# Kernel optimization log

Hardware: AMD Instinct MI355X
Metric: run time of the kernel (lower is better)

Reference implementation:

```python
import jax, jax.numpy as jnp
import numpy as np

N_NODES = 100000
N_EDGES = 3200000
IN_DIM = 32
HID = 64


def setup_inputs() -> dict:
    key = jax.random.key(0)
    ks = jax.random.split(key, 10)
    x = jax.random.normal(ks[0], (N_NODES, IN_DIM), dtype=jnp.float32)
    edge_index = jax.random.randint(ks[1], (2, N_EDGES), 0, N_NODES, dtype=jnp.int64)
    s = 0.1
    return {
        "x": x,
        "edge_index": edge_index,
        # SAGEConv layer 1: lin_l (neighbor path, with bias), lin_r (root path, no bias)
        "w1_l": jax.random.normal(ks[2], (HID, IN_DIM), dtype=jnp.float32) * s,
        "b1_l": jnp.zeros((HID,), dtype=jnp.float32),
        "w1_r": jax.random.normal(ks[3], (HID, IN_DIM), dtype=jnp.float32) * s,
        # SAGEConv layer 2
        "w2_l": jax.random.normal(ks[4], (HID, HID), dtype=jnp.float32) * s,
        "b2_l": jnp.zeros((HID,), dtype=jnp.float32),
        "w2_r": jax.random.normal(ks[5], (HID, HID), dtype=jnp.float32) * s,
        # final classifier Linear(hidden, 1)
        "w_cls": jax.random.normal(ks[6], (1, HID), dtype=jnp.float32) * s,
        "b_cls": jnp.zeros((1,), dtype=jnp.float32),
    }


def _sage_conv(h, src, dst, n_nodes, w_l, b_l, w_r):
    # mean-aggregate neighbor features (src -> dst), then lin_l(agg) + lin_r(h)
    msg = h[src]                                   # [E, F] gather
    agg = jax.ops.segment_sum(msg, dst, num_segments=n_nodes)
    cnt = jax.ops.segment_sum(jnp.ones((src.shape[0],), h.dtype), dst,
                              num_segments=n_nodes)
    mean = agg / jnp.maximum(cnt, 1.0)[:, None]    # [N, F]
    return mean @ w_l.T + b_l + h @ w_r.T


def reference(x, edge_index, w1_l, b1_l, w1_r, w2_l, b2_l, w2_r, w_cls, b_cls):
    src, dst = edge_index[0], edge_index[1]
    n = x.shape[0]
    h = _sage_conv(x, src, dst, n, w1_l, b1_l, w1_r)
    h = jax.nn.relu(h)  # dropout is identity at inference
    h = _sage_conv(h, src, dst, n, w2_l, b2_l, w2_r)
    h = jax.nn.relu(h)
    logits = h @ w_cls.T + b_cls                   # [N, 1]
    return jnp.squeeze(logits, -1)                 # [N]
```

## Files before the change

### kernel.cpp

```cpp
#include <hip/hip_runtime.h>

#define N_NODES 100000
#define N_EDGES 3200000
#define IN_DIM 32
#define HID 64
#define BSHIFT 8
#define BNODES 256
#define NB ((N_NODES + BNODES - 1) / BNODES)
#define NWG 256
#define CHUNK (N_EDGES / NWG)

typedef unsigned short u16;
typedef _Float16 h2 __attribute__((ext_vector_type(2)));
typedef _Float16 half8 __attribute__((ext_vector_type(8)));
typedef float float4v __attribute__((ext_vector_type(4)));

__device__ __forceinline__ h2 as_h2(unsigned u) {
  return __builtin_bit_cast(h2, u);
}
__device__ __forceinline__ unsigned as_u(h2 v) {
  return __builtin_bit_cast(unsigned, v);
}
__device__ __forceinline__ h2 shfl_xor_h2(h2 v, int m) {
  int i = __builtin_bit_cast(int, v);
  i = __shfl_xor(i, m, 64);
  return __builtin_bit_cast(h2, i);
}
__device__ __forceinline__ u16 f2h(float f) {
  _Float16 h = (_Float16)f;
  return __builtin_bit_cast(u16, h);
}
__device__ __forceinline__ unsigned scale_h2(unsigned u, float rinv) {
  h2 v = as_h2(u);
  h2 o;
  o.x = (_Float16)((float)v.x * rinv);
  o.y = (_Float16)((float)v.y * rinv);
  return as_u(o);
}

__global__ __launch_bounds__(256) void to_f16(
    const float* __restrict__ in, u16* __restrict__ outv, int n) {
  int i = blockIdx.x * 256 + threadIdx.x;
  if (i < n) outv[i] = f2h(in[i]);
}

__global__ __launch_bounds__(256) void prep_weights(
    const float* __restrict__ w1l, const float* __restrict__ w1r,
    const float* __restrict__ w2l, const float* __restrict__ w2r,
    u16* __restrict__ w1lf, u16* __restrict__ w1rf,
    u16* __restrict__ w2lf, u16* __restrict__ w2rf) {
  int i = blockIdx.x * 256 + threadIdx.x;
  if (i < HID * IN_DIM) {
    w1lf[i] = f2h(w1l[i]);
    w1rf[i] = f2h(w1r[i]);
  }
  if (i < HID * HID) {
    w2lf[i] = f2h(w2l[i]);
    w2rf[i] = f2h(w2r[i]);
  }
}

__global__ __launch_bounds__(256) void csr_count(
    const int* __restrict__ dst, int* __restrict__ counts) {
  __shared__ int h[NB];
  int w = blockIdx.x, tid = threadIdx.x;
  for (int i = tid; i < NB; i += 256) h[i] = 0;
  __syncthreads();
  int e0 = w * CHUNK;
  for (int i = tid; i < CHUNK; i += 256)
    atomicAdd(&h[dst[e0 + i] >> BSHIFT], 1);
  __syncthreads();
  for (int i = tid; i < NB; i += 256) counts[w * NB + i] = h[i];
}

__global__ __launch_bounds__(256) void csr_scan_w(
    int* __restrict__ counts, int* __restrict__ btot) {
  __shared__ int s[256];
  int b = blockIdx.x, tid = threadIdx.x;
  int v = counts[tid * NB + b];
  s[tid] = v;
  __syncthreads();
  for (int off = 1; off < 256; off <<= 1) {
    int t = (tid >= off) ? s[tid - off] : 0;
    __syncthreads();
    s[tid] += t;
    __syncthreads();
  }
  counts[tid * NB + b] = s[tid] - v;
  if (tid == 255) btot[b] = s[255];
}

__global__ __launch_bounds__(256) void csr_scan_b(
    const int* __restrict__ btot, int* __restrict__ bbase) {
  __shared__ int s[256];
  int tid = threadIdx.x;
  int g0 = tid * 2, g1 = tid * 2 + 1;
  int v0 = (g0 < NB) ? btot[g0] : 0;
  int v1 = (g1 < NB) ? btot[g1] : 0;
  int tsum = v0 + v1;
  s[tid] = tsum;
  __syncthreads();
  for (int off = 1; off < 256; off <<= 1) {
    int t = (tid >= off) ? s[tid - off] : 0;
    __syncthreads();
    s[tid] += t;
    __syncthreads();
  }
  int run = s[tid] - tsum;
  if (g0 < NB) bbase[g0] = run;
  if (g1 < NB) bbase[g1] = run + v0;
  if (tid == 0) bbase[NB] = N_EDGES;
}

__global__ __launch_bounds__(256) void csr_place(
    const int* __restrict__ src, const int* __restrict__ dst,
    const int* __restrict__ counts, const int* __restrict__ bbase,
    unsigned* __restrict__ staged) {
  __shared__ int cur[NB];
  int w = blockIdx.x, tid = threadIdx.x;
  for (int i = tid; i < NB; i += 256) cur[i] = bbase[i] + counts[w * NB + i];
  __syncthreads();
  int e0 = w * CHUNK;
  for (int i = tid; i < CHUNK; i += 256) {
    int d = dst[e0 + i];
    int b = d >> BSHIFT;
    int pos = atomicAdd(&cur[b], 1);
    staged[pos] = ((unsigned)src[e0 + i] << 8) | (unsigned)(d & (BNODES - 1));
  }
}

__global__ __launch_bounds__(256) void csr_fill(
    const unsigned* __restrict__ staged, const int* __restrict__ bbase,
    int* __restrict__ row_ptr, int* __restrict__ sorted_src) {
  __shared__ int s_cnt[BNODES];
  __shared__ int s_scan[BNODES];
  int b = blockIdx.x, tid = threadIdx.x;
  int n0 = b << BSHIFT;
  int beg = bbase[b], end = bbase[b + 1];
  s_cnt[tid] = 0;
  __syncthreads();
  for (int i = beg + tid; i < end; i += 256)
    atomicAdd(&s_cnt[staged[i] & (BNODES - 1)], 1);
  __syncthreads();
  int v = s_cnt[tid];
  s_scan[tid] = v;
  __syncthreads();
  for (int off = 1; off < BNODES; off <<= 1) {
    int t = (tid >= off) ? s_scan[tid - off] : 0;
    __syncthreads();
    s_scan[tid] += t;
    __syncthreads();
  }
  int excl = s_scan[tid] - v;
  int node = n0 + tid;
  if (node < N_NODES) row_ptr[node] = beg + excl;
  if (b == 0 && tid == 0) row_ptr[N_NODES] = N_EDGES;
  s_cnt[tid] = excl;
  __syncthreads();
  for (int i = beg + tid; i < end; i += 256) {
    unsigned p = staged[i];
    int r = atomicAdd(&s_cnt[p & (BNODES - 1)], 1);
    sorted_src[beg + r] = (int)(p >> 8);
  }
}

#define F1 72
__global__ __launch_bounds__(256) void layer1_fused(
    const u16* __restrict__ xh, const int* __restrict__ row_ptr,
    const int* __restrict__ sorted_src, const u16* __restrict__ w_lf,
    const float* __restrict__ b_l, const u16* __restrict__ w_rf,
    u16* __restrict__ h1h) {
  __shared__ __align__(16) u16 s_feat[16 * F1];

  int tid = threadIdx.x;
  int w = tid >> 6, lane = tid & 63;
  int q = lane & 3, g = lane >> 2;

  for (int m = 0; m < 4; ++m) {
    int nl = 4 * w + m;
    int node = blockIdx.x * 16 + nl;
    int rs = row_ptr[node];
    int deg = row_ptr[node + 1] - rs;
    h2 a0{}, a1{}, a2{}, a3{}, b0{}, b1{}, b2{}, b3{};
    int kk = g;
    for (; kk + 16 < deg; kk += 32) {
      int s0 = sorted_src[rs + kk];
      int s1 = sorted_src[rs + kk + 16];
      uint4 u0 = *(const uint4*)&xh[s0 * IN_DIM + 8 * q];
      uint4 u1 = *(const uint4*)&xh[s1 * IN_DIM + 8 * q];
      a0 += as_h2(u0.x); a1 += as_h2(u0.y); a2 += as_h2(u0.z); a3 += as_h2(u0.w);
      b0 += as_h2(u1.x); b1 += as_h2(u1.y); b2 += as_h2(u1.z); b3 += as_h2(u1.w);
    }
    if (kk < deg) {
      int s0 = sorted_src[rs + kk];
      uint4 u0 = *(const uint4*)&xh[s0 * IN_DIM + 8 * q];
      a0 += as_h2(u0.x); a1 += as_h2(u0.y); a2 += as_h2(u0.z); a3 += as_h2(u0.w);
    }
    a0 += b0; a1 += b1; a2 += b2; a3 += b3;
#pragma unroll
    for (int off = 4; off < 64; off <<= 1) {
      a0 += shfl_xor_h2(a0, off);
      a1 += shfl_xor_h2(a1, off);
      a2 += shfl_xor_h2(a2, off);
      a3 += shfl_xor_h2(a3, off);
    }
    if (g == 0) {
      float rinv = 1.0f / fmaxf((float)deg, 1.0f);
      uint4 o;
      o.x = scale_h2(as_u(a0), rinv);
      o.y = scale_h2(as_u(a1), rinv);
      o.z = scale_h2(as_u(a2), rinv);
      o.w = scale_h2(as_u(a3), rinv);
      *(uint4*)&s_feat[nl * F1 + 8 * q] = o;
    }
  }
  {
    int nm = lane >> 4, q2 = lane & 15;
    int nl = 4 * w + nm;
    int node = blockIdx.x * 16 + nl;
    unsigned ux = *(const unsigned*)&xh[node * IN_DIM + 2 * q2];
    *(unsigned*)&s_feat[nl * F1 + IN_DIM + 2 * q2] = ux;
  }
  __syncthreads();

  int q16 = lane & 15, g4 = lane >> 4;
  int j = 16 * w + q16;
  half8 b0f = *(const half8*)&w_lf[j * IN_DIM + 8 * g4];
  half8 b1f = *(const half8*)&w_rf[j * IN_DIM + 8 * g4];
  half8 a0f = *(const half8*)&s_feat[q16 * F1 + 8 * g4];
  half8 a1f = *(const half8*)&s_feat[q16 * F1 + 32 + 8 * g4];
  float4v acc = {};
  acc = __builtin_amdgcn_mfma_f32_16x16x32_f16(a0f, b0f, acc, 0, 0, 0);
  acc = __builtin_amdgcn_mfma_f32_16x16x32_f16(a1f, b1f, acc, 0, 0, 0);
  float bj = b_l[j];
#pragma unroll
  for (int reg = 0; reg < 4; ++reg) {
    int nl = 4 * g4 + reg;
    float v = fmaxf(acc[reg] + bj, 0.0f);
    h1h[(blockIdx.x * 16 + nl) * HID + j] = f2h(v);
  }
}

#define F2 136
__global__ __launch_bounds__(256) void layer2_fused(
    const u16* __restrict__ h1h, const int* __restrict__ row_ptr,
    const int* __restrict__ sorted_src, const u16* __restrict__ w_lf,
    const float* __restrict__ b_l, const u16* __restrict__ w_rf,
    const float* __restrict__ wc, const float* __restrict__ bc,
    float* __restrict__ out) {
  __shared__ __align__(16) u16 s_feat[16 * F2];
  __shared__ float s_out[16];

  int tid = threadIdx.x;
  if (tid < 16) s_out[tid] = bc[0];

  int w = tid >> 6, lane = tid & 63;
  int q = lane & 7, g = lane >> 3;

  for (int m = 0; m < 4; ++m) {
    int nl = 4 * w + m;
    int node = blockIdx.x * 16 + nl;
    int rs = row_ptr[node];
    int deg = row_ptr[node + 1] - rs;
    h2 a0{}, a1{}, a2{}, a3{}, b0{}, b1{}, b2{}, b3{};
    int kk = g;
    for (; kk + 8 < deg; kk += 16) {
      int s0 = sorted_src[rs + kk];
      int s1 = sorted_src[rs + kk + 8];
      uint4 u0 = *(const uint4*)&h1h[s0 * HID + 8 * q];
      uint4 u1 = *(const uint4*)&h1h[s1 * HID + 8 * q];
      a0 += as_h2(u0.x); a1 += as_h2(u0.y); a2 += as_h2(u0.z); a3 += as_h2(u0.w);
      b0 += as_h2(u1.x); b1 += as_h2(u1.y); b2 += as_h2(u1.z); b3 += as_h2(u1.w);
    }
    if (kk < deg) {
      int s0 = sorted_src[rs + kk];
      uint4 u0 = *(const uint4*)&h1h[s0 * HID + 8 * q];
      a0 += as_h2(u0.x); a1 += as_h2(u0.y); a2 += as_h2(u0.z); a3 += as_h2(u0.w);
    }
    a0 += b0; a1 += b1; a2 += b2; a3 += b3;
#pragma unroll
    for (int off = 8; off < 64; off <<= 1) {
      a0 += shfl_xor_h2(a0, off);
      a1 += shfl_xor_h2(a1, off);
      a2 += shfl_xor_h2(a2, off);
      a3 += shfl_xor_h2(a3, off);
    }
    if (g == 0) {
      float rinv = 1.0f / fmaxf((float)deg, 1.0f);
      uint4 o;
      o.x = scale_h2(as_u(a0), rinv);
      o.y = scale_h2(as_u(a1), rinv);
      o.z = scale_h2(as_u(a2), rinv);
      o.w = scale_h2(as_u(a3), rinv);
      *(uint4*)&s_feat[nl * F2 + 8 * q] = o;
    }
  }
  {
    int nm = lane >> 4, q2 = lane & 15;
    int nl = 4 * w + nm;
    int node = blockIdx.x * 16 + nl;
    uint2 uh = *(const uint2*)&h1h[node * HID + 4 * q2];
    *(uint2*)&s_feat[nl * F2 + HID + 4 * q2] = uh;
  }
  __syncthreads();

  int q16 = lane & 15, g4 = lane >> 4;
  int j = 16 * w + q16;
  half8 bf0 = *(const half8*)&w_lf[j * HID + 8 * g4];
  half8 bf1 = *(const half8*)&w_lf[j * HID + 32 + 8 * g4];
  half8 bf2 = *(const half8*)&w_rf[j * HID + 8 * g4];
  half8 bf3 = *(const half8*)&w_rf[j * HID + 32 + 8 * g4];
  float4v acc = {};
  acc = __builtin_amdgcn_mfma_f32_16x16x32_f16(
      *(const half8*)&s_feat[q16 * F2 + 8 * g4], bf0, acc, 0, 0, 0);
  acc = __builtin_amdgcn_mfma_f32_16x16x32_f16(
      *(const half8*)&s_feat[q16 * F2 + 32 + 8 * g4], bf1, acc, 0, 0, 0);
  acc = __builtin_amdgcn_mfma_f32_16x16x32_f16(
      *(const half8*)&s_feat[q16 * F2 + 64 + 8 * g4], bf2, acc, 0, 0, 0);
  acc = __builtin_amdgcn_mfma_f32_16x16x32_f16(
      *(const half8*)&s_feat[q16 * F2 + 96 + 8 * g4], bf3, acc, 0, 0, 0);
  float bj = b_l[j];
  float wcj = wc[j];
#pragma unroll
  for (int reg = 0; reg < 4; ++reg) {
    float v = fmaxf(acc[reg] + bj, 0.0f) * wcj;
    v += __shfl_xor(v, 1, 64);
    v += __shfl_xor(v, 2, 64);
    v += __shfl_xor(v, 4, 64);
    v += __shfl_xor(v, 8, 64);
    if (q16 == 0) atomicAdd(&s_out[4 * g4 + reg], v);
  }
  __syncthreads();
  if (tid < 16) out[blockIdx.x * 16 + tid] = s_out[tid];
}

extern "C" void kernel_launch(void* const* d_in, const int* in_sizes, int n_in,
                              void* d_out, int out_size, void* d_ws, size_t ws_size,
                              hipStream_t stream) {
  const float* x   = (const float*)d_in[0];
  const int*   ei  = (const int*)d_in[1];
  const float* w1l = (const float*)d_in[2];
  const float* b1l = (const float*)d_in[3];
  const float* w1r = (const float*)d_in[4];
  const float* w2l = (const float*)d_in[5];
  const float* b2l = (const float*)d_in[6];
  const float* w2r = (const float*)d_in[7];
  const float* wc  = (const float*)d_in[8];
  const float* bc  = (const float*)d_in[9];
  float* out = (float*)d_out;

  const int* src = ei;
  const int* dst = ei + N_EDGES;

  char* ws = (char*)d_ws;
  int*      row_ptr    = (int*)(ws + 0);
  int*      counts     = (int*)(ws + 400128);
  int*      btot       = (int*)(ws + 800768);
  int*      bbase      = (int*)(ws + 802560);
  unsigned* staged     = (unsigned*)(ws + 804352);
  int*      sorted_src = (int*)(ws + 13604352);
  u16*      xh         = (u16*)(ws + 26404352);
  u16*      h1h        = (u16*)(ws + 32804352);
  u16*      w1lf       = (u16*)(ws + 45604352);
  u16*      w1rf       = (u16*)(ws + 45608448);
  u16*      w2lf       = (u16*)(ws + 45612544);
  u16*      w2rf       = (u16*)(ws + 45620736);

  to_f16<<<(N_NODES * IN_DIM + 255) / 256, 256, 0, stream>>>(x, xh,
                                                             N_NODES * IN_DIM);
  prep_weights<<<(HID * HID + 255) / 256, 256, 0, stream>>>(
      w1l, w1r, w2l, w2r, w1lf, w1rf, w2lf, w2rf);
  csr_count<<<NWG, 256, 0, stream>>>(dst, counts);
  csr_scan_w<<<NB, 256, 0, stream>>>(counts, btot);
  csr_scan_b<<<1, 256, 0, stream>>>(btot, bbase);
  csr_place<<<NWG, 256, 0, stream>>>(src, dst, counts, bbase, staged);
  csr_fill<<<NB, 256, 0, stream>>>(staged, bbase, row_ptr, sorted_src);
  layer1_fused<<<N_NODES / 16, 256, 0, stream>>>(xh, row_ptr, sorted_src,
                                                 w1lf, b1l, w1rf, h1h);
  layer2_fused<<<N_NODES / 16, 256, 0, stream>>>(h1h, row_ptr, sorted_src,
                                                 w2lf, b2l, w2rf, wc, bc, out);
}
```

Baseline: 199.0 us.

## Interleave four nodes' neighbor gathers per wave and hoist weight loads

Each wave now gathers neighbors for its four nodes together in one loop bounded by the maximum degree, instead of handling the nodes one after another. This puts up to four independent gathers in flight per iteration, which raises memory-level parallelism and removes the serial per-node loop latency. Weight and bias loads are moved before the gather so they overlap with it, and launch bounds request 8 blocks per CU. The cost is more live registers for 16 accumulators, plus idle lanes on the divergent branches when the four degrees are unequal.

```diff
diff --git a/kernel.cpp b/kernel.cpp
--- a/kernel.cpp
+++ b/kernel.cpp
@@ -165,7 +165,7 @@
 }
 
 #define F1 72
-__global__ __launch_bounds__(256) void layer1_fused(
+__global__ __launch_bounds__(256, 8) void layer1_fused(
     const u16* __restrict__ xh, const int* __restrict__ row_ptr,
     const int* __restrict__ sorted_src, const u16* __restrict__ w_lf,
     const float* __restrict__ b_l, const u16* __restrict__ w_rf,
@@ -176,43 +176,75 @@
   int w = tid >> 6, lane = tid & 63;
   int q = lane & 3, g = lane >> 2;
 
-  for (int m = 0; m < 4; ++m) {
-    int nl = 4 * w + m;
-    int node = blockIdx.x * 16 + nl;
-    int rs = row_ptr[node];
-    int deg = row_ptr[node + 1] - rs;
-    h2 a0{}, a1{}, a2{}, a3{}, b0{}, b1{}, b2{}, b3{};
-    int kk = g;
-    for (; kk + 16 < deg; kk += 32) {
-      int s0 = sorted_src[rs + kk];
-      int s1 = sorted_src[rs + kk + 16];
-      uint4 u0 = *(const uint4*)&xh[s0 * IN_DIM + 8 * q];
-      uint4 u1 = *(const uint4*)&xh[s1 * IN_DIM + 8 * q];
-      a0 += as_h2(u0.x); a1 += as_h2(u0.y); a2 += as_h2(u0.z); a3 += as_h2(u0.w);
-      b0 += as_h2(u1.x); b1 += as_h2(u1.y); b2 += as_h2(u1.z); b3 += as_h2(u1.w);
-    }
-    if (kk < deg) {
-      int s0 = sorted_src[rs + kk];
-      uint4 u0 = *(const uint4*)&xh[s0 * IN_DIM + 8 * q];
-      a0 += as_h2(u0.x); a1 += as_h2(u0.y); a2 += as_h2(u0.z); a3 += as_h2(u0.w);
-    }
-    a0 += b0; a1 += b1; a2 += b2; a3 += b3;
+  int q16 = lane & 15, g4 = lane >> 4;
+  int j = 16 * w + q16;
+  half8 b0f = *(const half8*)&w_lf[j * IN_DIM + 8 * g4];
+  half8 b1f = *(const half8*)&w_rf[j * IN_DIM + 8 * g4];
+  float bj = b_l[j];
+
+  int nbase = blockIdx.x * 16 + 4 * w;
+  int r0 = row_ptr[nbase + 0], r1 = row_ptr[nbase + 1];
+  int r2 = row_ptr[nbase + 2], r3 = row_ptr[nbase + 3];
+  int r4 = row_ptr[nbase + 4];
+  int d0 = r1 - r0, d1 = r2 - r1, d2 = r3 - r2, d3 = r4 - r3;
+  int dmax = max(max(d0, d1), max(d2, d3));
+
+  h2 A0{}, A1{}, A2{}, A3{};
+  h2 B0{}, B1{}, B2{}, B3{};
+  h2 C0{}, C1{}, C2{}, C3{};
+  h2 D0{}, D1{}, D2{}, D3{};
+  for (int kk = g; kk < dmax; kk += 16) {
+    if (kk < d0) {
+      int s = sorted_src[r0 + kk];
+      uint4 u = *(const uint4*)&xh[s * IN_DIM + 8 * q];
+      A0 += as_h2(u.x); A1 += as_h2(u.y); A2 += as_h2(u.z); A3 += as_h2(u.w);
+    }
+    if (kk < d1) {
+      int s = sorted_src[r1 + kk];
+      uint4 u = *(const uint4*)&xh[s * IN_DIM + 8 * q];
+      B0 += as_h2(u.x); B1 += as_h2(u.y); B2 += as_h2(u.z); B3 += as_h2(u.w);
+    }
+    if (kk < d2) {
+      int s = sorted_src[r2 + kk];
+      uint4 u = *(const uint4*)&xh[s * IN_DIM + 8 * q];
+      C0 += as_h2(u.x); C1 += as_h2(u.y); C2 += as_h2(u.z); C3 += as_h2(u.w);
+    }
+    if (kk < d3) {
+      int s = sorted_src[r3 + kk];
+      uint4 u = *(const uint4*)&xh[s * IN_DIM + 8 * q];
+      D0 += as_h2(u.x); D1 += as_h2(u.y); D2 += as_h2(u.z); D3 += as_h2(u.w);
+    }
+  }
 #pragma unroll
-    for (int off = 4; off < 64; off <<= 1) {
-      a0 += shfl_xor_h2(a0, off);
-      a1 += shfl_xor_h2(a1, off);
-      a2 += shfl_xor_h2(a2, off);
-      a3 += shfl_xor_h2(a3, off);
-    }
-    if (g == 0) {
-      float rinv = 1.0f / fmaxf((float)deg, 1.0f);
-      uint4 o;
-      o.x = scale_h2(as_u(a0), rinv);
-      o.y = scale_h2(as_u(a1), rinv);
-      o.z = scale_h2(as_u(a2), rinv);
-      o.w = scale_h2(as_u(a3), rinv);
-      *(uint4*)&s_feat[nl * F1 + 8 * q] = o;
-    }
+  for (int off = 4; off < 64; off <<= 1) {
+    A0 += shfl_xor_h2(A0, off); A1 += shfl_xor_h2(A1, off);
+    A2 += shfl_xor_h2(A2, off); A3 += shfl_xor_h2(A3, off);
+    B0 += shfl_xor_h2(B0, off); B1 += shfl_xor_h2(B1, off);
+    B2 += shfl_xor_h2(B2, off); B3 += shfl_xor_h2(B3, off);
+    C0 += shfl_xor_h2(C0, off); C1 += shfl_xor_h2(C1, off);
+    C2 += shfl_xor_h2(C2, off); C3 += shfl_xor_h2(C3, off);
+    D0 += shfl_xor_h2(D0, off); D1 += shfl_xor_h2(D1, off);
+    D2 += shfl_xor_h2(D2, off); D3 += shfl_xor_h2(D3, off);
+  }
+  if (g == 0) {
+    int nl = 4 * w;
+    float ri0 = 1.0f / fmaxf((float)d0, 1.0f);
+    float ri1 = 1.0f / fmaxf((float)d1, 1.0f);
+    float ri2 = 1.0f / fmaxf((float)d2, 1.0f);
+    float ri3 = 1.0f / fmaxf((float)d3, 1.0f);
+    uint4 o;
+    o.x = scale_h2(as_u(A0), ri0); o.y = scale_h2(as_u(A1), ri0);
+    o.z = scale_h2(as_u(A2), ri0); o.w = scale_h2(as_u(A3), ri0);
+    *(uint4*)&s_feat[(nl + 0) * F1 + 8 * q] = o;
+    o.x = scale_h2(as_u(B0), ri1); o.y = scale_h2(as_u(B1), ri1);
+    o.z = scale_h2(as_u(B2), ri1); o.w = scale_h2(as_u(B3), ri1);
+    *(uint4*)&s_feat[(nl + 1) * F1 + 8 * q] = o;
+    o.x = scale_h2(as_u(C0), ri2); o.y = scale_h2(as_u(C1), ri2);
+    o.z = scale_h2(as_u(C2), ri2); o.w = scale_h2(as_u(C3), ri2);
+    *(uint4*)&s_feat[(nl + 2) * F1 + 8 * q] = o;
+    o.x = scale_h2(as_u(D0), ri3); o.y = scale_h2(as_u(D1), ri3);
+    o.z = scale_h2(as_u(D2), ri3); o.w = scale_h2(as_u(D3), ri3);
+    *(uint4*)&s_feat[(nl + 3) * F1 + 8 * q] = o;
   }
   {
     int nm = lane >> 4, q2 = lane & 15;
@@ -223,16 +255,11 @@
   }
   __syncthreads();
 
-  int q16 = lane & 15, g4 = lane >> 4;
-  int j = 16 * w + q16;
-  half8 b0f = *(const half8*)&w_lf[j * IN_DIM + 8 * g4];
-  half8 b1f = *(const half8*)&w_rf[j * IN_DIM + 8 * g4];
   half8 a0f = *(const half8*)&s_feat[q16 * F1 + 8 * g4];
   half8 a1f = *(const half8*)&s_feat[q16 * F1 + 32 + 8 * g4];
   float4v acc = {};
   acc = __builtin_amdgcn_mfma_f32_16x16x32_f16(a0f, b0f, acc, 0, 0, 0);
   acc = __builtin_amdgcn_mfma_f32_16x16x32_f16(a1f, b1f, acc, 0, 0, 0);
-  float bj = b_l[j];
 #pragma unroll
   for (int reg = 0; reg < 4; ++reg) {
     int nl = 4 * g4 + reg;
@@ -242,7 +269,7 @@
 }
 
 #define F2 136
-__global__ __launch_bounds__(256) void layer2_fused(
+__global__ __launch_bounds__(256, 8) void layer2_fused(
     const u16* __restrict__ h1h, const int* __restrict__ row_ptr,
     const int* __restrict__ sorted_src, const u16* __restrict__ w_lf,
     const float* __restrict__ b_l, const u16* __restrict__ w_rf,
@@ -257,43 +284,78 @@
   int w = tid >> 6, lane = tid & 63;
   int q = lane & 7, g = lane >> 3;
 
-  for (int m = 0; m < 4; ++m) {
-    int nl = 4 * w + m;
-    int node = blockIdx.x * 16 + nl;
-    int rs = row_ptr[node];
-    int deg = row_ptr[node + 1] - rs;
-    h2 a0{}, a1{}, a2{}, a3{}, b0{}, b1{}, b2{}, b3{};
-    int kk = g;
-    for (; kk + 8 < deg; kk += 16) {
-      int s0 = sorted_src[rs + kk];
-      int s1 = sorted_src[rs + kk + 8];
-      uint4 u0 = *(const uint4*)&h1h[s0 * HID + 8 * q];
-      uint4 u1 = *(const uint4*)&h1h[s1 * HID + 8 * q];
-      a0 += as_h2(u0.x); a1 += as_h2(u0.y); a2 += as_h2(u0.z); a3 += as_h2(u0.w);
-      b0 += as_h2(u1.x); b1 += as_h2(u1.y); b2 += as_h2(u1.z); b3 += as_h2(u1.w);
-    }
-    if (kk < deg) {
-      int s0 = sorted_src[rs + kk];
-      uint4 u0 = *(const uint4*)&h1h[s0 * HID + 8 * q];
-      a0 += as_h2(u0.x); a1 += as_h2(u0.y); a2 += as_h2(u0.z); a3 += as_h2(u0.w);
-    }
-    a0 += b0; a1 += b1; a2 += b2; a3 += b3;
+  int q16 = lane & 15, g4 = lane >> 4;
+  int j = 16 * w + q16;
+  half8 bf0 = *(const half8*)&w_lf[j * HID + 8 * g4];
+  half8 bf1 = *(const half8*)&w_lf[j * HID + 32 + 8 * g4];
+  half8 bf2 = *(const half8*)&w_rf[j * HID + 8 * g4];
+  half8 bf3 = *(const half8*)&w_rf[j * HID + 32 + 8 * g4];
+  float bj = b_l[j];
+  float wcj = wc[j];
+
+  int nbase = blockIdx.x * 16 + 4 * w;
+  int r0 = row_ptr[nbase + 0], r1 = row_ptr[nbase + 1];
+  int r2 = row_ptr[nbase + 2], r3 = row_ptr[nbase + 3];
+  int r4 = row_ptr[nbase + 4];
+  int d0 = r1 - r0, d1 = r2 - r1, d2 = r3 - r2, d3 = r4 - r3;
+  int dmax = max(max(d0, d1), max(d2, d3));
+
+  h2 A0{}, A1{}, A2{}, A3{};
+  h2 B0{}, B1{}, B2{}, B3{};
+  h2 C0{}, C1{}, C2{}, C3{};
+  h2 D0{}, D1{}, D2{}, D3{};
+  for (int kk = g; kk < dmax; kk += 8) {
+    if (kk < d0) {
+      int s = sorted_src[r0 + kk];
+      uint4 u = *(const uint4*)&h1h[s * HID + 8 * q];
+      A0 += as_h2(u.x); A1 += as_h2(u.y); A2 += as_h2(u.z); A3 += as_h2(u.w);
+    }
+    if (kk < d1) {
+      int s = sorted_src[r1 + kk];
+      uint4 u = *(const uint4*)&h1h[s * HID + 8 * q];
+      B0 += as_h2(u.x); B1 += as_h2(u.y); B2 += as_h2(u.z); B3 += as_h2(u.w);
+    }
+    if (kk < d2) {
+      int s = sorted_src[r2 + kk];
+      uint4 u = *(const uint4*)&h1h[s * HID + 8 * q];
+      C0 += as_h2(u.x); C1 += as_h2(u.y); C2 += as_h2(u.z); C3 += as_h2(u.w);
+    }
+    if (kk < d3) {
+      int s = sorted_src[r3 + kk];
+      uint4 u = *(const uint4*)&h1h[s * HID + 8 * q];
+      D0 += as_h2(u.x); D1 += as_h2(u.y); D2 += as_h2(u.z); D3 += as_h2(u.w);
+    }
+  }
 #pragma unroll
-    for (int off = 8; off < 64; off <<= 1) {
-      a0 += shfl_xor_h2(a0, off);
-      a1 += shfl_xor_h2(a1, off);
-      a2 += shfl_xor_h2(a2, off);
-      a3 += shfl_xor_h2(a3, off);
-    }
-    if (g == 0) {
-      float rinv = 1.0f / fmaxf((float)deg, 1.0f);
-      uint4 o;
-      o.x = scale_h2(as_u(a0), rinv);
-      o.y = scale_h2(as_u(a1), rinv);
-      o.z = scale_h2(as_u(a2), rinv);
-      o.w = scale_h2(as_u(a3), rinv);
-      *(uint4*)&s_feat[nl * F2 + 8 * q] = o;
-    }
+  for (int off = 8; off < 64; off <<= 1) {
+    A0 += shfl_xor_h2(A0, off); A1 += shfl_xor_h2(A1, off);
+    A2 += shfl_xor_h2(A2, off); A3 += shfl_xor_h2(A3, off);
+    B0 += shfl_xor_h2(B0, off); B1 += shfl_xor_h2(B1, off);
+    B2 += shfl_xor_h2(B2, off); B3 += shfl_xor_h2(B3, off);
+    C0 += shfl_xor_h2(C0, off); C1 += shfl_xor_h2(C1, off);
+    C2 += shfl_xor_h2(C2, off); C3 += shfl_xor_h2(C3, off);
+    D0 += shfl_xor_h2(D0, off); D1 += shfl_xor_h2(D1, off);
+    D2 += shfl_xor_h2(D2, off); D3 += shfl_xor_h2(D3, off);
+  }
+  if (g == 0) {
+    int nl = 4 * w;
+    float ri0 = 1.0f / fmaxf((float)d0, 1.0f);
+    float ri1 = 1.0f / fmaxf((float)d1, 1.0f);
+    float ri2 = 1.0f / fmaxf((float)d2, 1.0f);
+    float ri3 = 1.0f / fmaxf((float)d3, 1.0f);
+    uint4 o;
+    o.x = scale_h2(as_u(A0), ri0); o.y = scale_h2(as_u(A1), ri0);
+    o.z = scale_h2(as_u(A2), ri0); o.w = scale_h2(as_u(A3), ri0);
+    *(uint4*)&s_feat[(nl + 0) * F2 + 8 * q] = o;
+    o.x = scale_h2(as_u(B0), ri1); o.y = scale_h2(as_u(B1), ri1);
+    o.z = scale_h2(as_u(B2), ri1); o.w = scale_h2(as_u(B3), ri1);
+    *(uint4*)&s_feat[(nl + 1) * F2 + 8 * q] = o;
+    o.x = scale_h2(as_u(C0), ri2); o.y = scale_h2(as_u(C1), ri2);
+    o.z = scale_h2(as_u(C2), ri2); o.w = scale_h2(as_u(C3), ri2);
+    *(uint4*)&s_feat[(nl + 2) * F2 + 8 * q] = o;
+    o.x = scale_h2(as_u(D0), ri3); o.y = scale_h2(as_u(D1), ri3);
+    o.z = scale_h2(as_u(D2), ri3); o.w = scale_h2(as_u(D3), ri3);
+    *(uint4*)&s_feat[(nl + 3) * F2 + 8 * q] = o;
   }
   {
     int nm = lane >> 4, q2 = lane & 15;
@@ -304,12 +366,6 @@
   }
   __syncthreads();
 
-  int q16 = lane & 15, g4 = lane >> 4;
-  int j = 16 * w + q16;
-  half8 bf0 = *(const half8*)&w_lf[j * HID + 8 * g4];
-  half8 bf1 = *(const half8*)&w_lf[j * HID + 32 + 8 * g4];
-  half8 bf2 = *(const half8*)&w_rf[j * HID + 8 * g4];
-  half8 bf3 = *(const half8*)&w_rf[j * HID + 32 + 8 * g4];
   float4v acc = {};
   acc = __builtin_amdgcn_mfma_f32_16x16x32_f16(
       *(const half8*)&s_feat[q16 * F2 + 8 * g4], bf0, acc, 0, 0, 0);
@@ -319,8 +375,6 @@
       *(const half8*)&s_feat[q16 * F2 + 64 + 8 * g4], bf2, acc, 0, 0, 0);
   acc = __builtin_amdgcn_mfma_f32_16x16x32_f16(
       *(const half8*)&s_feat[q16 * F2 + 96 + 8 * g4], bf3, acc, 0, 0, 0);
-  float bj = b_l[j];
-  float wcj = wc[j];
 #pragma unroll
   for (int reg = 0; reg < 4; ++reg) {
     float v = fmaxf(acc[reg] + bj, 0.0f) * wcj;
```

Result: slower. 214.4 us (+7.8%).

## Use finer CSR buckets and more partition workgroups in edge sort

Applied to the files above, without the earlier changes.

The CSR construction now uses 64-node buckets (1563 buckets) and 1024 partitioning workgroups instead of 256-node buckets and 256 workgroups. The two scan kernels are reworked so each thread handles 4 workgroups or 8 buckets, and csr_fill only uses 64 threads for its per-node scan. The intent is more parallelism in the count and place passes, with smaller, better-spread fill blocks. The cost is a larger counts matrix, more LDS atomics per workgroup, and a relocated workspace layout.

```diff
diff --git a/kernel.cpp b/kernel.cpp
--- a/kernel.cpp
+++ b/kernel.cpp
@@ -4,10 +4,10 @@
 #define N_EDGES 3200000
 #define IN_DIM 32
 #define HID 64
-#define BSHIFT 8
-#define BNODES 256
+#define BSHIFT 6
+#define BNODES 64
 #define NB ((N_NODES + BNODES - 1) / BNODES)
-#define NWG 256
+#define NWG 1024
 #define CHUNK (N_EDGES / NWG)
 
 typedef unsigned short u16;
@@ -77,8 +77,14 @@
     int* __restrict__ counts, int* __restrict__ btot) {
   __shared__ int s[256];
   int b = blockIdx.x, tid = threadIdx.x;
-  int v = counts[tid * NB + b];
-  s[tid] = v;
+  int v[4];
+  int tsum = 0;
+#pragma unroll
+  for (int i = 0; i < 4; ++i) {
+    v[i] = counts[(4 * tid + i) * NB + b];
+    tsum += v[i];
+  }
+  s[tid] = tsum;
   __syncthreads();
   for (int off = 1; off < 256; off <<= 1) {
     int t = (tid >= off) ? s[tid - off] : 0;
@@ -86,7 +92,12 @@
     s[tid] += t;
     __syncthreads();
   }
-  counts[tid * NB + b] = s[tid] - v;
+  int run = s[tid] - tsum;
+#pragma unroll
+  for (int i = 0; i < 4; ++i) {
+    counts[(4 * tid + i) * NB + b] = run;
+    run += v[i];
+  }
   if (tid == 255) btot[b] = s[255];
 }
 
@@ -94,10 +105,15 @@
     const int* __restrict__ btot, int* __restrict__ bbase) {
   __shared__ int s[256];
   int tid = threadIdx.x;
-  int g0 = tid * 2, g1 = tid * 2 + 1;
-  int v0 = (g0 < NB) ? btot[g0] : 0;
-  int v1 = (g1 < NB) ? btot[g1] : 0;
-  int tsum = v0 + v1;
+  int base = tid * 8;
+  int v[8];
+  int tsum = 0;
+#pragma unroll
+  for (int i = 0; i < 8; ++i) {
+    int g = base + i;
+    v[i] = (g < NB) ? btot[g] : 0;
+    tsum += v[i];
+  }
   s[tid] = tsum;
   __syncthreads();
   for (int off = 1; off < 256; off <<= 1) {
@@ -107,8 +123,12 @@
     __syncthreads();
   }
   int run = s[tid] - tsum;
-  if (g0 < NB) bbase[g0] = run;
-  if (g1 < NB) bbase[g1] = run + v0;
+#pragma unroll
+  for (int i = 0; i < 8; ++i) {
+    int g = base + i;
+    if (g < NB) bbase[g] = run;
+    run += v[i];
+  }
   if (tid == 0) bbase[NB] = N_EDGES;
 }
 
@@ -125,7 +145,8 @@
     int d = dst[e0 + i];
     int b = d >> BSHIFT;
     int pos = atomicAdd(&cur[b], 1);
-    staged[pos] = ((unsigned)src[e0 + i] << 8) | (unsigned)(d & (BNODES - 1));
+    staged[pos] = ((unsigned)src[e0 + i] << BSHIFT) |
+                  (unsigned)(d & (BNODES - 1));
   }
 }
 
@@ -137,30 +158,31 @@
   int b = blockIdx.x, tid = threadIdx.x;
   int n0 = b << BSHIFT;
   int beg = bbase[b], end = bbase[b + 1];
-  s_cnt[tid] = 0;
+  if (tid < BNODES) s_cnt[tid] = 0;
   __syncthreads();
   for (int i = beg + tid; i < end; i += 256)
     atomicAdd(&s_cnt[staged[i] & (BNODES - 1)], 1);
   __syncthreads();
-  int v = s_cnt[tid];
-  s_scan[tid] = v;
+  if (tid < BNODES) s_scan[tid] = s_cnt[tid];
   __syncthreads();
   for (int off = 1; off < BNODES; off <<= 1) {
-    int t = (tid >= off) ? s_scan[tid - off] : 0;
-    __syncthreads();
-    s_scan[tid] += t;
-    __syncthreads();
-  }
-  int excl = s_scan[tid] - v;
-  int node = n0 + tid;
-  if (node < N_NODES) row_ptr[node] = beg + excl;
+    int t = (tid < BNODES && tid >= off) ? s_scan[tid - off] : 0;
+    __syncthreads();
+    if (tid < BNODES) s_scan[tid] += t;
+    __syncthreads();
+  }
+  if (tid < BNODES) {
+    int node = n0 + tid;
+    int excl = s_scan[tid] - s_cnt[tid];
+    if (node < N_NODES) row_ptr[node] = beg + excl;
+    s_cnt[tid] = excl;
+  }
   if (b == 0 && tid == 0) row_ptr[N_NODES] = N_EDGES;
-  s_cnt[tid] = excl;
   __syncthreads();
   for (int i = beg + tid; i < end; i += 256) {
     unsigned p = staged[i];
     int r = atomicAdd(&s_cnt[p & (BNODES - 1)], 1);
-    sorted_src[beg + r] = (int)(p >> 8);
+    sorted_src[beg + r] = (int)(p >> BSHIFT);
   }
 }
 
@@ -181,7 +203,8 @@
     int node = blockIdx.x * 16 + nl;
     int rs = row_ptr[node];
     int deg = row_ptr[node + 1] - rs;
-    h2 a0{}, a1{}, a2{}, a3{}, b0{}, b1{}, b2{}, b3{};
+    h2 a0{}, a1{}, a2{}, a3{};
+    h2 b0{}, b1{}, b2{}, b3{};
     int kk = g;
     for (; kk + 16 < deg; kk += 32) {
       int s0 = sorted_src[rs + kk];
@@ -262,7 +285,8 @@
     int node = blockIdx.x * 16 + nl;
     int rs = row_ptr[node];
     int deg = row_ptr[node + 1] - rs;
-    h2 a0{}, a1{}, a2{}, a3{}, b0{}, b1{}, b2{}, b3{};
+    h2 a0{}, a1{}, a2{}, a3{};
+    h2 b0{}, b1{}, b2{}, b3{};
     int kk = g;
     for (; kk + 8 < deg; kk += 16) {
       int s0 = sorted_src[rs + kk];
@@ -355,16 +379,16 @@
   char* ws = (char*)d_ws;
   int*      row_ptr    = (int*)(ws + 0);
   int*      counts     = (int*)(ws + 400128);
-  int*      btot       = (int*)(ws + 800768);
-  int*      bbase      = (int*)(ws + 802560);
-  unsigned* staged     = (unsigned*)(ws + 804352);
-  int*      sorted_src = (int*)(ws + 13604352);
-  u16*      xh         = (u16*)(ws + 26404352);
-  u16*      h1h        = (u16*)(ws + 32804352);
-  u16*      w1lf       = (u16*)(ws + 45604352);
-  u16*      w1rf       = (u16*)(ws + 45608448);
-  u16*      w2lf       = (u16*)(ws + 45612544);
-  u16*      w2rf       = (u16*)(ws + 45620736);
+  int*      btot       = (int*)(ws + 6802176);
+  int*      bbase      = (int*)(ws + 6808576);
+  unsigned* staged     = (unsigned*)(ws + 6815232);
+  int*      sorted_src = (int*)(ws + 19615232);
+  u16*      xh         = (u16*)(ws + 32415232);
+  u16*      h1h        = (u16*)(ws + 38815232);
+  u16*      w1lf       = (u16*)(ws + 51615232);
+  u16*      w1rf       = (u16*)(ws + 51619328);
+  u16*      w2lf       = (u16*)(ws + 51623424);
+  u16*      w2rf       = (u16*)(ws + 51631616);
 
   to_f16<<<(N_NODES * IN_DIM + 255) / 256, 256, 0, stream>>>(x, xh,
                                                              N_NODES * IN_DIM);
```

Result: slower. 215.6 us (+8.4%).
